# Kernel optimization log

Hardware: AMD Instinct MI355X
Metric: run time of the kernel (lower is better)

The kernel has to match this reference:

```python
import jax, jax.numpy as jnp
import numpy as np

B, S, D, H = 2, 2048, 1024, 16
HD = D // H  # head dim = 64

def setup_inputs() -> dict:
    key = jax.random.key(0)
    ks = jax.random.split(key, 3)
    scale = 1.0 / np.sqrt(D)
    return {
        "x": jax.random.normal(ks[0], (B, S, D), jnp.float32),
        "W_attn": jax.random.normal(ks[1], (D, 3 * D), jnp.float32) * scale,
        "b_attn": jnp.zeros((3 * D,), jnp.float32),
        "W_proj": jax.random.normal(ks[2], (D, D), jnp.float32) * scale,
        "b_proj": jnp.zeros((D,), jnp.float32),
    }

def reference(x, W_attn, b_attn, W_proj, b_proj):
    b, s, d = x.shape
    qkv = x @ W_attn + b_attn                      # [B,S,3D]
    q, k, v = jnp.split(qkv, 3, axis=-1)
    # [B,S,D] -> [B,H,S,HD]
    def heads(t):
        return t.reshape(b, s, H, HD).transpose(0, 2, 1, 3)
    q, k, v = heads(q), heads(k), heads(v)
    scores = jnp.einsum('bhqd,bhkd->bhqk', q, k) * (1.0 / np.sqrt(HD))
    causal = jnp.tril(jnp.ones((s, s), dtype=bool))
    scores = jnp.where(causal[None, None], scores, -jnp.inf)
    probs = jax.nn.softmax(scores, axis=-1)
    y = jnp.einsum('bhqk,bhkd->bhqd', probs, v)    # [B,H,S,HD]
    y = y.transpose(0, 2, 1, 3).reshape(b, s, d)
    return y @ W_proj + b_proj
```

## Files before the change

kernel.cpp:

```cpp
#include <hip/hip_runtime.h>

typedef __bf16 bf16;
typedef __bf16 bf16x4 __attribute__((ext_vector_type(4)));
typedef __bf16 bf16x8 __attribute__((ext_vector_type(8)));
typedef float f32x4 __attribute__((ext_vector_type(4)));

#define S_LEN 2048
#define D_DIM 1024
#define N_HEAD 16
#define HEAD_DIM 64
#define M_TOK 4096
#define BH 32

#define EXP2F(x) __builtin_amdgcn_exp2f(x)
#define Q_SCALE 0.18033688f

#define SW(r, c) ((c) ^ (((r) & 3) << 4))
#define SIG(r) (((r) & 0x23) | (((r) & 0x04) << 2) | (((r) & 0x18) >> 1))

typedef __attribute__((address_space(3))) void lds_void;
typedef const __attribute__((address_space(1))) void gbl_void;

__device__ __forceinline__ void gl_lds16(const bf16* g, bf16* l) {
  __builtin_amdgcn_global_load_lds((gbl_void*)g, (lds_void*)l, 16, 0, 0);
}

__global__ __launch_bounds__(256) void k_cast(const float* __restrict__ x,
                                              bf16* __restrict__ o, int n) {
  int i = (blockIdx.x * 256 + threadIdx.x) * 4;
  if (i >= n) return;
  float4 v = *(const float4*)(x + i);
  bf16x4 w;
  w[0] = (bf16)v.x; w[1] = (bf16)v.y; w[2] = (bf16)v.z; w[3] = (bf16)v.w;
  *(bf16x4*)(o + i) = w;
}

__global__ __launch_bounds__(256) void k_transpose(const float* __restrict__ W,
                                                   bf16* __restrict__ Wt,
                                                   int K, int N) {
  __shared__ float tile[32][33];
  int nb = blockIdx.x, kb = blockIdx.y;
  int t = threadIdx.x;
  int r = t >> 3, c4 = (t & 7) * 4;
  float4 v = *(const float4*)&W[(kb * 32 + r) * N + nb * 32 + c4];
  tile[r][c4 + 0] = v.x; tile[r][c4 + 1] = v.y;
  tile[r][c4 + 2] = v.z; tile[r][c4 + 3] = v.w;
  __syncthreads();
  bf16x4 o;
  #pragma unroll
  for (int i = 0; i < 4; i++) o[i] = (bf16)tile[c4 + i][r];
  *(bf16x4*)&Wt[(nb * 32 + r) * K + kb * 32 + c4] = o;
}

__global__ __launch_bounds__(256, 2)
void k_gemm_qkv(const bf16* __restrict__ A, const bf16* __restrict__ Bt,
                const float* __restrict__ bias,
                bf16* __restrict__ qk, bf16* __restrict__ vT) {
  __shared__ bf16 As[128 * 32];
  __shared__ bf16 Bs[128 * 32];
  const int K = 1024;
  int bn = blockIdx.x, bm = blockIdx.y;
  int t = threadIdx.x;
  int wave = t >> 6, lane = t & 63, c = lane & 15, quad = lane >> 4;
  int wm = wave & 1, wn = wave >> 1;
  int ldrow = lane >> 2, ldcol = (lane & 3) * 8;

  const bf16* Ag = A + (size_t)(bm * 128) * K;
  const bf16* Bg = Bt + (size_t)(bn * 128) * K;

  f32x4 acc[4][4] = {};

  for (int k0 = 0; k0 < K; k0 += 32) {
    __syncthreads();
    #pragma unroll
    for (int q = 0; q < 2; q++) {
      int r0 = (wave * 2 + q) * 16;
      gl_lds16(&Ag[(size_t)(r0 + ldrow) * K + k0 + ldcol], &As[r0 * 32]);
      gl_lds16(&Bg[(size_t)(r0 + ldrow) * K + k0 + ldcol], &Bs[r0 * 32]);
    }
    __syncthreads();
    bf16x8 af[4];
    #pragma unroll
    for (int mt = 0; mt < 4; mt++)
      af[mt] = *(const bf16x8*)&As[(wm * 64 + mt * 16 + c) * 32 + quad * 8];
    #pragma unroll
    for (int nt = 0; nt < 4; nt++) {
      bf16x8 bfr = *(const bf16x8*)&Bs[(wn * 64 + nt * 16 + c) * 32 + quad * 8];
      #pragma unroll
      for (int mt = 0; mt < 4; mt++)
        acc[mt][nt] = __builtin_amdgcn_mfma_f32_16x16x32_bf16(af[mt], bfr, acc[mt][nt], 0, 0, 0);
    }
  }

  #pragma unroll
  for (int nt = 0; nt < 4; nt++) {
    int n = bn * 128 + wn * 64 + nt * 16 + c;
    int which = n >> 10, nl = n & 1023;
    int h = nl >> 6, hd = nl & 63;
    float bv = bias[n];
    #pragma unroll
    for (int mt = 0; mt < 4; mt++) {
      int m0 = bm * 128 + wm * 64 + mt * 16 + quad * 4;
      int b = m0 >> 11, s0 = m0 & 2047;
      int bh = b * N_HEAD + h;
      if (which == 2) {
        bf16x4 o;
        #pragma unroll
        for (int r = 0; r < 4; r++) o[r] = (bf16)(acc[mt][nt][r] + bv);
        *(bf16x4*)&vT[((size_t)bh * HEAD_DIM + hd) * S_LEN + s0] = o;
      } else if (which == 0) {
        #pragma unroll
        for (int r = 0; r < 4; r++)
          qk[(bh * S_LEN + s0 + r) * HEAD_DIM + hd] = (bf16)((acc[mt][nt][r] + bv) * Q_SCALE);
      } else {
        #pragma unroll
        for (int r = 0; r < 4; r++)
          qk[BH * S_LEN * HEAD_DIM + (bh * S_LEN + s0 + r) * HEAD_DIM + hd] = (bf16)(acc[mt][nt][r] + bv);
      }
    }
  }
}

__global__ __launch_bounds__(256, 4)
void k_attn(const bf16* __restrict__ qk, const bf16* __restrict__ vT,
            bf16* __restrict__ y) {
  __shared__ bf16 Ks[2][64][64];
  __shared__ bf16 Vs[2][64][64];
  int bx = blockIdx.x;
  int bh = bx & 31;
  int tile = 31 - (bx >> 5);
  int t = threadIdx.x, w = t >> 6, lane = t & 63, c = lane & 15, quad = lane >> 4;
  const bf16* Qg = qk + (size_t)bh * (S_LEN * HEAD_DIM);
  const bf16* Kg = qk + (size_t)(BH + bh) * (S_LEN * HEAD_DIM);
  const bf16* Vg = vT + (size_t)bh * (HEAD_DIM * S_LEN);
  int b = bh >> 4, h = bh & 15;
  int srow = t >> 3, scol = (t & 7) * 8;
  int swcol = SW(srow, scol);
  int sigr = SIG(srow);

  const int nkb = tile + 1;
  const int dthr = w * 16 + c;

  bf16x8 qf[2];
  f32x4 acc[4] = {};
  float mM = -1e30f, lL = 0.f;
  {
    int qr = tile * 64 + w * 16 + c;
    qf[0] = *(const bf16x8*)&Qg[qr * HEAD_DIM + quad * 8];
    qf[1] = *(const bf16x8*)&Qg[qr * HEAD_DIM + 32 + quad * 8];
  }

  bf16x8 kr0 = *(const bf16x8*)&Kg[srow * HEAD_DIM + scol];
  bf16x8 kr1 = *(const bf16x8*)&Kg[(srow + 32) * HEAD_DIM + scol];
  bf16x8 vr0 = *(const bf16x8*)&Vg[(size_t)srow * S_LEN + scol];
  bf16x8 vr1 = *(const bf16x8*)&Vg[(size_t)(srow + 32) * S_LEN + scol];
  *(bf16x8*)&Ks[0][sigr][swcol] = kr0;
  *(bf16x8*)&Ks[0][sigr + 32][swcol] = kr1;
  *(bf16x8*)&Vs[0][srow][swcol] = vr0;
  *(bf16x8*)&Vs[0][srow + 32][swcol] = vr1;

  for (int kb = 0; kb < nkb; kb++) {
    __syncthreads();
    int cur = kb & 1;
    bool haveNext = (kb + 1 < nkb);
    if (haveNext) {
      kr0 = *(const bf16x8*)&Kg[((kb + 1) * 64 + srow) * HEAD_DIM + scol];
      kr1 = *(const bf16x8*)&Kg[((kb + 1) * 64 + srow + 32) * HEAD_DIM + scol];
      vr0 = *(const bf16x8*)&Vg[(size_t)srow * S_LEN + (kb + 1) * 64 + scol];
      vr1 = *(const bf16x8*)&Vg[(size_t)(srow + 32) * S_LEN + (kb + 1) * 64 + scol];
    }

    bool dia = (kb == tile);

    f32x4 sc[4];
    #pragma unroll
    for (int kt = 0; kt < 4; kt++) {
      int kr = kt * 16 + c;
      bf16x8 kf0 = *(const bf16x8*)&Ks[cur][kr][SW(kr, quad * 8)];
      bf16x8 kf1 = *(const bf16x8*)&Ks[cur][kr][SW(kr, 32 + quad * 8)];
      f32x4 z = {};
      z = __builtin_amdgcn_mfma_f32_16x16x32_bf16(kf0, qf[0], z, 0, 0, 0);
      z = __builtin_amdgcn_mfma_f32_16x16x32_bf16(kf1, qf[1], z, 0, 0, 0);
      sc[kt] = z;
    }

    if (dia) {
      #pragma unroll
      for (int kt = 0; kt < 4; kt++) {
        int kbase = (kt >> 1) * 32 + quad * 8 + (kt & 1) * 4;
        #pragma unroll
        for (int r = 0; r < 4; r++)
          if (kbase + r > dthr) sc[kt][r] = -1e30f;
      }
    }

    bf16x8 pf[2];
    {
      float mx = sc[0][0];
      #pragma unroll
      for (int kt = 0; kt < 4; kt++)
        #pragma unroll
        for (int r = 0; r < 4; r++) mx = fmaxf(mx, sc[kt][r]);
      mx = fmaxf(mx, __shfl_xor(mx, 16));
      mx = fmaxf(mx, __shfl_xor(mx, 32));
      float mnew = fmaxf(mM, mx);
      float alpha = EXP2F(mM - mnew);
      float sum = 0.f;
      #pragma unroll
      for (int kt = 0; kt < 4; kt++) {
        #pragma unroll
        for (int r = 0; r < 4; r++) {
          float pv = EXP2F(sc[kt][r] - mnew);
          sum += pv;
          pf[kt >> 1][(kt & 1) * 4 + r] = (bf16)pv;
        }
      }
      sum += __shfl_xor(sum, 16);
      sum += __shfl_xor(sum, 32);
      lL = lL * alpha + sum;
      mM = mnew;
      #pragma unroll
      for (int dt = 0; dt < 4; dt++)
        #pragma unroll
        for (int r = 0; r < 4; r++) acc[dt][r] *= alpha;
    }

    #pragma unroll
    for (int ks = 0; ks < 2; ks++) {
      #pragma unroll
      for (int dt = 0; dt < 4; dt++) {
        int vrow = dt * 16 + c;
        bf16x8 vf = *(const bf16x8*)&Vs[cur][vrow][SW(vrow, ks * 32 + quad * 8)];
        acc[dt] = __builtin_amdgcn_mfma_f32_16x16x32_bf16(vf, pf[ks], acc[dt], 0, 0, 0);
      }
    }

    if (haveNext) {
      int nxt = cur ^ 1;
      *(bf16x8*)&Ks[nxt][sigr][swcol] = kr0;
      *(bf16x8*)&Ks[nxt][sigr + 32][swcol] = kr1;
      *(bf16x8*)&Vs[nxt][srow][swcol] = vr0;
      *(bf16x8*)&Vs[nxt][srow + 32][swcol] = vr1;
    }
  }

  {
    int q = tile * 64 + w * 16 + c;
    float linv = 1.0f / lL;
    #pragma unroll
    for (int dt = 0; dt < 4; dt++) {
      bf16x4 o;
      #pragma unroll
      for (int r = 0; r < 4; r++) o[r] = (bf16)(acc[dt][r] * linv);
      *(bf16x4*)&y[((size_t)(b * S_LEN + q) * N_HEAD + h) * HEAD_DIM + dt * 16 + quad * 4] = o;
    }
  }
}

__global__ __launch_bounds__(256, 2)
void k_gemm_proj(const bf16* __restrict__ A, const bf16* __restrict__ Bt,
                 const float* __restrict__ bias, float* __restrict__ out) {
  __shared__ bf16 As[128 * 32];
  __shared__ bf16 Bs[64 * 32];
  const int K = 1024;
  int bn = blockIdx.x, bm = blockIdx.y;
  int t = threadIdx.x;
  int wave = t >> 6, lane = t & 63, c = lane & 15, quad = lane >> 4;
  int wm = wave & 1, wn = wave >> 1;
  int ldrow = lane >> 2, ldcol = (lane & 3) * 8;

  const bf16* Ag = A + (size_t)(bm * 128) * K;
  const bf16* Bg = Bt + (size_t)(bn * 64) * K;

  f32x4 acc[4][2] = {};

  for (int k0 = 0; k0 < K; k0 += 32) {
    __syncthreads();
    #pragma unroll
    for (int q = 0; q < 2; q++) {
      int r0 = (wave * 2 + q) * 16;
      gl_lds16(&Ag[(size_t)(r0 + ldrow) * K + k0 + ldcol], &As[r0 * 32]);
    }
    gl_lds16(&Bg[(size_t)(wave * 16 + ldrow) * K + k0 + ldcol], &Bs[wave * 16 * 32]);
    __syncthreads();
    bf16x8 af[4];
    #pragma unroll
    for (int mt = 0; mt < 4; mt++)
      af[mt] = *(const bf16x8*)&As[(wm * 64 + mt * 16 + c) * 32 + quad * 8];
    #pragma unroll
    for (int nt = 0; nt < 2; nt++) {
      bf16x8 bfr = *(const bf16x8*)&Bs[(wn * 32 + nt * 16 + c) * 32 + quad * 8];
      #pragma unroll
      for (int mt = 0; mt < 4; mt++)
        acc[mt][nt] = __builtin_amdgcn_mfma_f32_16x16x32_bf16(af[mt], bfr, acc[mt][nt], 0, 0, 0);
    }
  }

  #pragma unroll
  for (int nt = 0; nt < 2; nt++) {
    int n = bn * 64 + wn * 32 + nt * 16 + c;
    float bv = bias[n];
    #pragma unroll
    for (int mt = 0; mt < 4; mt++) {
      #pragma unroll
      for (int r = 0; r < 4; r++) {
        int m = bm * 128 + wm * 64 + mt * 16 + quad * 4 + r;
        out[(size_t)m * D_DIM + n] = acc[mt][nt][r] + bv;
      }
    }
  }
}

extern "C" void kernel_launch(void* const* d_in, const int* in_sizes, int n_in,
                              void* d_out, int out_size, void* d_ws, size_t ws_size,
                              hipStream_t stream) {
  const float* x      = (const float*)d_in[0];
  const float* W_attn = (const float*)d_in[1];
  const float* b_attn = (const float*)d_in[2];
  const float* W_proj = (const float*)d_in[3];
  const float* b_proj = (const float*)d_in[4];
  float* out = (float*)d_out;

  bf16* x_bf = (bf16*)d_ws;
  bf16* wat  = x_bf + 4096 * 1024;
  bf16* wpt  = wat + 3072 * 1024;
  bf16* qk   = wpt + 1024 * 1024;
  bf16* vT   = qk + 8 * 1024 * 1024;
  bf16* y_bf = vT + 4 * 1024 * 1024;

  k_cast<<<4096, 256, 0, stream>>>(x, x_bf, 4096 * 1024);
  k_transpose<<<dim3(3072 / 32, 1024 / 32), 256, 0, stream>>>(W_attn, wat, 1024, 3072);
  k_transpose<<<dim3(1024 / 32, 1024 / 32), 256, 0, stream>>>(W_proj, wpt, 1024, 1024);
  k_gemm_qkv<<<dim3(24, 32), 256, 0, stream>>>(x_bf, wat, b_attn, qk, vT);
  k_attn<<<1024, 256, 0, stream>>>(qk, vT, y_bf);
  k_gemm_proj<<<dim3(16, 32), 256, 0, stream>>>(y_bf, wpt, b_proj, out);
}
```

Before: 184.4 us.

## Pair causal query tiles per attention block to balance work and share K/V loads

The attention kernel now uses 512-thread blocks, each handling two query tiles (p and 31-p) of the same head with two 4-wave strips. Every block does the same total of 33 key-tile iterations, and one K/V LDS stage serves both strips. The goal is to remove causal load imbalance and halve K/V global traffic per query tile. It also adds s_setprio around the MFMA sections. In exchange, the short-tile strip idles at barriers once its causal range is done, and only half as many blocks are launched.

```diff
diff --git a/kernel.cpp b/kernel.cpp
--- a/kernel.cpp
+++ b/kernel.cpp
@@ -121,15 +121,17 @@
   }
 }
 
-__global__ __launch_bounds__(256, 4)
+__global__ __launch_bounds__(512, 4)
 void k_attn(const bf16* __restrict__ qk, const bf16* __restrict__ vT,
             bf16* __restrict__ y) {
   __shared__ bf16 Ks[2][64][64];
   __shared__ bf16 Vs[2][64][64];
   int bx = blockIdx.x;
   int bh = bx & 31;
-  int tile = 31 - (bx >> 5);
+  int p = bx >> 5;
   int t = threadIdx.x, w = t >> 6, lane = t & 63, c = lane & 15, quad = lane >> 4;
+  int strip = w >> 2, wr = w & 3;
+  int myTile = strip ? (31 - p) : p;
   const bf16* Qg = qk + (size_t)bh * (S_LEN * HEAD_DIM);
   const bf16* Kg = qk + (size_t)(BH + bh) * (S_LEN * HEAD_DIM);
   const bf16* Vg = vT + (size_t)bh * (HEAD_DIM * S_LEN);
@@ -138,114 +140,114 @@
   int swcol = SW(srow, scol);
   int sigr = SIG(srow);
 
-  const int nkb = tile + 1;
-  const int dthr = w * 16 + c;
+  const int nkb = 32 - p;
+  const int myLast = strip ? (31 - p) : p;
+  const int dthr = wr * 16 + c;
 
   bf16x8 qf[2];
   f32x4 acc[4] = {};
   float mM = -1e30f, lL = 0.f;
   {
-    int qr = tile * 64 + w * 16 + c;
+    int qr = myTile * 64 + wr * 16 + c;
     qf[0] = *(const bf16x8*)&Qg[qr * HEAD_DIM + quad * 8];
     qf[1] = *(const bf16x8*)&Qg[qr * HEAD_DIM + 32 + quad * 8];
   }
 
-  bf16x8 kr0 = *(const bf16x8*)&Kg[srow * HEAD_DIM + scol];
-  bf16x8 kr1 = *(const bf16x8*)&Kg[(srow + 32) * HEAD_DIM + scol];
-  bf16x8 vr0 = *(const bf16x8*)&Vg[(size_t)srow * S_LEN + scol];
-  bf16x8 vr1 = *(const bf16x8*)&Vg[(size_t)(srow + 32) * S_LEN + scol];
-  *(bf16x8*)&Ks[0][sigr][swcol] = kr0;
-  *(bf16x8*)&Ks[0][sigr + 32][swcol] = kr1;
-  *(bf16x8*)&Vs[0][srow][swcol] = vr0;
-  *(bf16x8*)&Vs[0][srow + 32][swcol] = vr1;
+  bf16x8 kr = *(const bf16x8*)&Kg[srow * HEAD_DIM + scol];
+  bf16x8 vr = *(const bf16x8*)&Vg[(size_t)srow * S_LEN + scol];
+  *(bf16x8*)&Ks[0][sigr][swcol] = kr;
+  *(bf16x8*)&Vs[0][srow][swcol] = vr;
 
   for (int kb = 0; kb < nkb; kb++) {
     __syncthreads();
     int cur = kb & 1;
     bool haveNext = (kb + 1 < nkb);
     if (haveNext) {
-      kr0 = *(const bf16x8*)&Kg[((kb + 1) * 64 + srow) * HEAD_DIM + scol];
-      kr1 = *(const bf16x8*)&Kg[((kb + 1) * 64 + srow + 32) * HEAD_DIM + scol];
-      vr0 = *(const bf16x8*)&Vg[(size_t)srow * S_LEN + (kb + 1) * 64 + scol];
-      vr1 = *(const bf16x8*)&Vg[(size_t)(srow + 32) * S_LEN + (kb + 1) * 64 + scol];
-    }
-
-    bool dia = (kb == tile);
-
-    f32x4 sc[4];
-    #pragma unroll
-    for (int kt = 0; kt < 4; kt++) {
-      int kr = kt * 16 + c;
-      bf16x8 kf0 = *(const bf16x8*)&Ks[cur][kr][SW(kr, quad * 8)];
-      bf16x8 kf1 = *(const bf16x8*)&Ks[cur][kr][SW(kr, 32 + quad * 8)];
-      f32x4 z = {};
-      z = __builtin_amdgcn_mfma_f32_16x16x32_bf16(kf0, qf[0], z, 0, 0, 0);
-      z = __builtin_amdgcn_mfma_f32_16x16x32_bf16(kf1, qf[1], z, 0, 0, 0);
-      sc[kt] = z;
-    }
-
-    if (dia) {
+      kr = *(const bf16x8*)&Kg[((kb + 1) * 64 + srow) * HEAD_DIM + scol];
+      vr = *(const bf16x8*)&Vg[(size_t)srow * S_LEN + (kb + 1) * 64 + scol];
+    }
+
+    bool act = (kb <= myLast);
+    if (act) {
+      bool dia = (kb == myLast);
+
+      f32x4 sc[4];
+      __builtin_amdgcn_s_setprio(1);
       #pragma unroll
       for (int kt = 0; kt < 4; kt++) {
-        int kbase = (kt >> 1) * 32 + quad * 8 + (kt & 1) * 4;
-        #pragma unroll
-        for (int r = 0; r < 4; r++)
-          if (kbase + r > dthr) sc[kt][r] = -1e30f;
-      }
-    }
-
-    bf16x8 pf[2];
-    {
-      float mx = sc[0][0];
-      #pragma unroll
-      for (int kt = 0; kt < 4; kt++)
-        #pragma unroll
-        for (int r = 0; r < 4; r++) mx = fmaxf(mx, sc[kt][r]);
-      mx = fmaxf(mx, __shfl_xor(mx, 16));
-      mx = fmaxf(mx, __shfl_xor(mx, 32));
-      float mnew = fmaxf(mM, mx);
-      float alpha = EXP2F(mM - mnew);
-      float sum = 0.f;
-      #pragma unroll
-      for (int kt = 0; kt < 4; kt++) {
-        #pragma unroll
-        for (int r = 0; r < 4; r++) {
-          float pv = EXP2F(sc[kt][r] - mnew);
-          sum += pv;
-          pf[kt >> 1][(kt & 1) * 4 + r] = (bf16)pv;
+        int krr = kt * 16 + c;
+        bf16x8 kf0 = *(const bf16x8*)&Ks[cur][krr][SW(krr, quad * 8)];
+        bf16x8 kf1 = *(const bf16x8*)&Ks[cur][krr][SW(krr, 32 + quad * 8)];
+        f32x4 z = {};
+        z = __builtin_amdgcn_mfma_f32_16x16x32_bf16(kf0, qf[0], z, 0, 0, 0);
+        z = __builtin_amdgcn_mfma_f32_16x16x32_bf16(kf1, qf[1], z, 0, 0, 0);
+        sc[kt] = z;
+      }
+      __builtin_amdgcn_s_setprio(0);
+
+      if (dia) {
+        #pragma unroll
+        for (int kt = 0; kt < 4; kt++) {
+          int kbase = (kt >> 1) * 32 + quad * 8 + (kt & 1) * 4;
+          #pragma unroll
+          for (int r = 0; r < 4; r++)
+            if (kbase + r > dthr) sc[kt][r] = -1e30f;
         }
       }
-      sum += __shfl_xor(sum, 16);
-      sum += __shfl_xor(sum, 32);
-      lL = lL * alpha + sum;
-      mM = mnew;
-      #pragma unroll
-      for (int dt = 0; dt < 4; dt++)
-        #pragma unroll
-        for (int r = 0; r < 4; r++) acc[dt][r] *= alpha;
-    }
-
-    #pragma unroll
-    for (int ks = 0; ks < 2; ks++) {
-      #pragma unroll
-      for (int dt = 0; dt < 4; dt++) {
-        int vrow = dt * 16 + c;
-        bf16x8 vf = *(const bf16x8*)&Vs[cur][vrow][SW(vrow, ks * 32 + quad * 8)];
-        acc[dt] = __builtin_amdgcn_mfma_f32_16x16x32_bf16(vf, pf[ks], acc[dt], 0, 0, 0);
-      }
+
+      bf16x8 pf[2];
+      {
+        float mx = sc[0][0];
+        #pragma unroll
+        for (int kt = 0; kt < 4; kt++)
+          #pragma unroll
+          for (int r = 0; r < 4; r++) mx = fmaxf(mx, sc[kt][r]);
+        mx = fmaxf(mx, __shfl_xor(mx, 16));
+        mx = fmaxf(mx, __shfl_xor(mx, 32));
+        float mnew = fmaxf(mM, mx);
+        float alpha = EXP2F(mM - mnew);
+        float sum = 0.f;
+        #pragma unroll
+        for (int kt = 0; kt < 4; kt++) {
+          #pragma unroll
+          for (int r = 0; r < 4; r++) {
+            float pv = EXP2F(sc[kt][r] - mnew);
+            sum += pv;
+            pf[kt >> 1][(kt & 1) * 4 + r] = (bf16)pv;
+          }
+        }
+        sum += __shfl_xor(sum, 16);
+        sum += __shfl_xor(sum, 32);
+        lL = lL * alpha + sum;
+        mM = mnew;
+        #pragma unroll
+        for (int dt = 0; dt < 4; dt++)
+          #pragma unroll
+          for (int r = 0; r < 4; r++) acc[dt][r] *= alpha;
+      }
+
+      __builtin_amdgcn_s_setprio(1);
+      #pragma unroll
+      for (int ks = 0; ks < 2; ks++) {
+        #pragma unroll
+        for (int dt = 0; dt < 4; dt++) {
+          int vrow = dt * 16 + c;
+          bf16x8 vf = *(const bf16x8*)&Vs[cur][vrow][SW(vrow, ks * 32 + quad * 8)];
+          acc[dt] = __builtin_amdgcn_mfma_f32_16x16x32_bf16(vf, pf[ks], acc[dt], 0, 0, 0);
+        }
+      }
+      __builtin_amdgcn_s_setprio(0);
     }
 
     if (haveNext) {
       int nxt = cur ^ 1;
-      *(bf16x8*)&Ks[nxt][sigr][swcol] = kr0;
-      *(bf16x8*)&Ks[nxt][sigr + 32][swcol] = kr1;
-      *(bf16x8*)&Vs[nxt][srow][swcol] = vr0;
-      *(bf16x8*)&Vs[nxt][srow + 32][swcol] = vr1;
+      *(bf16x8*)&Ks[nxt][sigr][swcol] = kr;
+      *(bf16x8*)&Vs[nxt][srow][swcol] = vr;
     }
   }
 
   {
-    int q = tile * 64 + w * 16 + c;
+    int q = myTile * 64 + wr * 16 + c;
     float linv = 1.0f / lL;
     #pragma unroll
     for (int dt = 0; dt < 4; dt++) {
@@ -332,6 +334,6 @@
   k_transpose<<<dim3(3072 / 32, 1024 / 32), 256, 0, stream>>>(W_attn, wat, 1024, 3072);
   k_transpose<<<dim3(1024 / 32, 1024 / 32), 256, 0, stream>>>(W_proj, wpt, 1024, 1024);
   k_gemm_qkv<<<dim3(24, 32), 256, 0, stream>>>(x_bf, wat, b_attn, qk, vT);
-  k_attn<<<1024, 256, 0, stream>>>(qk, vT, y_bf);
+  k_attn<<<512, 512, 0, stream>>>(qk, vT, y_bf);
   k_gemm_proj<<<dim3(16, 32), 256, 0, stream>>>(y_bf, wpt, b_proj, out);
 }
```

New measurement: 181.7 us. No clear change (-1.4%).
